# Optimization experiments

Hardware: AMD Instinct MI355X
Metric: run time of the kernel (lower is better)

Reference implementation:

```python
import jax, jax.numpy as jnp
import numpy as np

N_NODES, N_EDGES, N_GRAPHS = 50000, 500000, 64
NODE_D, EDGE_D, GLOB_D = 256, 128, 64
EPS = 1e-5


def setup_inputs() -> dict:
    key = jax.random.key(0)
    ks = jax.random.split(key, 12)
    inp = {
        "x": jax.random.normal(ks[0], (N_NODES, NODE_D), jnp.float32),
        "edge_attr": jax.random.normal(ks[1], (N_EDGES, EDGE_D), jnp.float32),
        "u": jax.random.normal(ks[2], (N_GRAPHS, GLOB_D), jnp.float32),
        "W1": jax.random.normal(ks[3], (NODE_D + EDGE_D, 4 * EDGE_D), jnp.float32) * 0.02,
        "b1": jnp.zeros((4 * EDGE_D,), jnp.float32),
        "W2": jax.random.normal(ks[4], (4 * EDGE_D, EDGE_D), jnp.float32) * 0.02,
        "b2": jnp.zeros((EDGE_D,), jnp.float32),
        "W3": jax.random.normal(ks[5], (NODE_D + EDGE_D + GLOB_D, 4 * NODE_D), jnp.float32) * 0.02,
        "b3": jnp.zeros((4 * NODE_D,), jnp.float32),
        "W4": jax.random.normal(ks[6], (4 * NODE_D, NODE_D), jnp.float32) * 0.02,
        "b4": jnp.zeros((NODE_D,), jnp.float32),
        "gamma": jnp.ones((NODE_D,), jnp.float32),
        "beta": jnp.zeros((NODE_D,), jnp.float32),
        "edge_index": jax.random.randint(ks[7], (2, N_EDGES), 0, N_NODES, jnp.int64 if jax.config.jax_enable_x64 else jnp.int32),
        "batch": jnp.sort(jax.random.randint(ks[8], (N_NODES,), 0, N_GRAPHS, jnp.int64 if jax.config.jax_enable_x64 else jnp.int32)),
    }
    return inp


def reference(x, edge_attr, u, W1, b1, W2, b2, W3, b3, W4, b4, gamma, beta, edge_index, batch):
    row, col = edge_index[0], edge_index[1]
    n = x.shape[0]
    # edge MLP on [x[row] || edge_attr]
    e = jnp.concatenate([x[row], edge_attr], axis=1)            # [E, node+edge]
    e = jnp.maximum(e @ W1 + b1, 0.0) @ W2 + b2                 # [E, edge]
    # scatter-mean by destination node
    s = jax.ops.segment_sum(e, col, num_segments=n)             # [N, edge]
    cnt = jax.ops.segment_sum(jnp.ones((col.shape[0],), x.dtype), col, num_segments=n)
    agg = s / jnp.maximum(cnt, 1.0)[:, None]
    # node update MLP on [x || agg || u[batch]]
    h = jnp.concatenate([x, agg, u[batch]], axis=1)             # [N, node+edge+glob]
    h = jnp.maximum(h @ W3 + b3, 0.0) @ W4 + b4                 # [N, node]
    # residual + layernorm (dropout p=0 -> identity)
    y = h + x
    mu = jnp.mean(y, axis=-1, keepdims=True)
    var = jnp.mean((y - mu) ** 2, axis=-1, keepdims=True)
    return (y - mu) * jax.lax.rsqrt(var + EPS) * gamma + beta
```

## Files before the change

kernel.cpp:

```cpp
#include <hip/hip_runtime.h>
#include <stdint.h>

#define NE 500000
#define NN 50000
#define ND 256
#define ED 128
#define GD 64
#define MAXDEG 64

typedef float f4v __attribute__((ext_vector_type(4)));
typedef short s8v __attribute__((ext_vector_type(8)));
typedef short s4v __attribute__((ext_vector_type(4)));

static __device__ __forceinline__ short f2bf(float f) {
  union { float f; uint32_t u; } v; v.f = f;
  uint32_t r = v.u + 0x7FFFu + ((v.u >> 16) & 1u);
  return (short)(r >> 16);
}
static __device__ __forceinline__ float bf2f(uint32_t u) {
  union { uint32_t u; float f; } v; v.u = u << 16; return v.f;
}

static __device__ __forceinline__ void gload_lds16(const void* g, void* l) {
  __builtin_amdgcn_global_load_lds(
      (const __attribute__((address_space(1))) unsigned int*)g,
      (__attribute__((address_space(3))) unsigned int*)l,
      16, 0, 0);
}

static __device__ __forceinline__ void pack_one(const float* __restrict__ src,
                                                short* __restrict__ dst, int C, int idx) {
  int k = idx / C, c = idx - k * C;
  int ks = k >> 5, kh = (k >> 3) & 3, j = k & 7;
  dst[(((ks * C + c) * 4 + kh) << 3) + j] = f2bf(src[idx]);
}

#define J5 500000
#define J0 3200000
#define J1 196608
#define J2 65536
#define J3 458752
#define J4 262144
__global__ void prep_kernel(const float* __restrict__ x, short* __restrict__ xbf,
                            const float* __restrict__ W1, const float* __restrict__ W2,
                            const float* __restrict__ W3, const float* __restrict__ W4,
                            short* __restrict__ w1p, short* __restrict__ w2p,
                            short* __restrict__ w3p, short* __restrict__ w4p,
                            const int* __restrict__ ecol, unsigned int* __restrict__ cnt,
                            int* __restrict__ elist) {
  int idx = blockIdx.x * blockDim.x + threadIdx.x;
  if (idx < J5) {
    int c = ecol[idx];
    unsigned int slot = atomicAdd(&cnt[c], 1u);
    if (slot < MAXDEG) elist[c * MAXDEG + slot] = idx;
    return;
  }
  idx -= J5;
  if (idx < J0) {
    int i = idx * 4;
    const float4 v = *(const float4*)(x + i);
    s4v o; o[0] = f2bf(v.x); o[1] = f2bf(v.y); o[2] = f2bf(v.z); o[3] = f2bf(v.w);
    *(s4v*)(xbf + i) = o;
    return;
  }
  idx -= J0;
  if (idx < J1) { pack_one(W1, w1p, 512, idx); return; }
  idx -= J1;
  if (idx < J2) { pack_one(W2, w2p, 128, idx); return; }
  idx -= J2;
  if (idx < J3) { pack_one(W3, w3p, 1024, idx); return; }
  idx -= J3;
  if (idx < J4) { pack_one(W4, w4p, 256, idx); return; }
}

__global__ void agg_kernel(const unsigned short* __restrict__ ebuf,
                           const int* __restrict__ elist,
                           const unsigned int* __restrict__ cnt,
                           unsigned short* __restrict__ aggbf) {
  int tid = threadIdx.x;
  int lane = tid & 63;
  int node = blockIdx.x * 4 + (tid >> 6);
  if (node >= NN) return;
  unsigned int deg = cnt[node];
  unsigned int jend = deg < MAXDEG ? deg : MAXDEG;
  const int jg = lane >> 4;
  const int ch = lane & 15;
  float a[8] = {0.f, 0.f, 0.f, 0.f, 0.f, 0.f, 0.f, 0.f};
  const int* el = elist + (size_t)node * MAXDEG;
  for (unsigned int j = jg; j < jend; j += 4) {
    int eid = el[j];
    s8v v = *(const s8v*)(ebuf + (size_t)eid * ED + ch * 8);
    #pragma unroll
    for (int i = 0; i < 8; ++i) a[i] += bf2f((uint32_t)(uint16_t)v[i]);
  }
  #pragma unroll
  for (int d = 16; d < 64; d <<= 1) {
    #pragma unroll
    for (int i = 0; i < 8; ++i) a[i] += __shfl_xor(a[i], d);
  }
  if (jg == 0) {
    float rc = 1.0f / (deg > 0 ? (float)deg : 1.0f);
    s8v o;
    #pragma unroll
    for (int i = 0; i < 8; ++i) o[i] = f2bf(a[i] * rc);
    *(s8v*)(aggbf + (size_t)node * ED + ch * 8) = o;
  }
}

__launch_bounds__(1024, 4)
__global__ void edge_kernel(const short* __restrict__ xbf,
                            const float* __restrict__ edge_attr,
                            const short* __restrict__ w1p,
                            const float* __restrict__ b1,
                            const short* __restrict__ w2p,
                            const float* __restrict__ b2,
                            const int* __restrict__ erow,
                            unsigned short* __restrict__ ebuf) {
  __shared__ __align__(16) short smem[81920];
  char* const Xb = (char*)smem;
  char* const Eb = (char*)smem + 65536;
  char* const Hb = (char*)smem + 98304;
  const int tid = threadIdx.x;
  const int lane = tid & 63;
  const int w = tid >> 6;
  const int lh = lane >> 4;
  const int ll = lane & 15;
  const int e0 = blockIdx.x * 128;

  {
    #pragma unroll
    for (int i = 0; i < 4; ++i) {
      int p = w * 4 + i;
      int row = 2 * p + (lane >> 5);
      int rid = erow[e0 + row];
      int cg = (lane & 31) ^ (row & 7);
      gload_lds16(xbf + (size_t)rid * 256 + cg * 8, Xb + p * 1024);
    }
  }

  #pragma unroll
  for (int it = 0; it < 2; ++it) {
    int id = tid + it * 1024;
    int row = id >> 4, oct = id & 15;
    s8v vals = {0, 0, 0, 0, 0, 0, 0, 0};
    if (e0 + row < NE) {
      const float* p = edge_attr + (size_t)(e0 + row) * ED + oct * 8;
      const float4 v0 = *(const float4*)(p);
      const float4 v1 = *(const float4*)(p + 4);
      vals[0] = f2bf(v0.x); vals[1] = f2bf(v0.y); vals[2] = f2bf(v0.z); vals[3] = f2bf(v0.w);
      vals[4] = f2bf(v1.x); vals[5] = f2bf(v1.y); vals[6] = f2bf(v1.z); vals[7] = f2bf(v1.w);
    }
    *(s8v*)(Eb + row * 256 + ((oct ^ (row & 7)) << 4)) = vals;
  }
  __syncthreads();

  f4v acc1[2][8];
  #pragma unroll
  for (int n = 0; n < 2; ++n)
    #pragma unroll
    for (int m = 0; m < 8; ++m)
      acc1[n][m] = (f4v){0.f, 0.f, 0.f, 0.f};

  for (int ks = 0; ks < 8; ++ks) {
    s8v wf0 = *(const s8v*)(w1p + (((ks * 512 + w * 16 + ll) * 4 + lh) << 3));
    s8v wf1 = *(const s8v*)(w1p + (((ks * 512 + 256 + w * 16 + ll) * 4 + lh) << 3));
    #pragma unroll
    for (int mh = 0; mh < 2; ++mh) {
      s8v hf[4];
      #pragma unroll
      for (int m = 0; m < 4; ++m) {
        int row = 64 * mh + 16 * m + ll;
        int byte = row * 512 + (((ks * 4 + lh) ^ (row & 7)) << 4);
        hf[m] = *(const s8v*)(Xb + byte);
      }
      #pragma unroll
      for (int m = 0; m < 4; ++m) {
        acc1[0][4 * mh + m] = __builtin_amdgcn_mfma_f32_16x16x32_bf16(wf0, hf[m], acc1[0][4 * mh + m], 0, 0, 0);
        acc1[1][4 * mh + m] = __builtin_amdgcn_mfma_f32_16x16x32_bf16(wf1, hf[m], acc1[1][4 * mh + m], 0, 0, 0);
      }
    }
  }
  for (int ks = 8; ks < 12; ++ks) {
    s8v wf0 = *(const s8v*)(w1p + (((ks * 512 + w * 16 + ll) * 4 + lh) << 3));
    s8v wf1 = *(const s8v*)(w1p + (((ks * 512 + 256 + w * 16 + ll) * 4 + lh) << 3));
    #pragma unroll
    for (int mh = 0; mh < 2; ++mh) {
      s8v hf[4];
      #pragma unroll
      for (int m = 0; m < 4; ++m) {
        int row = 64 * mh + 16 * m + ll;
        int byte = row * 256 + ((((ks - 8) * 4 + lh) ^ (row & 7)) << 4);
        hf[m] = *(const s8v*)(Eb + byte);
      }
      #pragma unroll
      for (int m = 0; m < 4; ++m) {
        acc1[0][4 * mh + m] = __builtin_amdgcn_mfma_f32_16x16x32_bf16(wf0, hf[m], acc1[0][4 * mh + m], 0, 0, 0);
        acc1[1][4 * mh + m] = __builtin_amdgcn_mfma_f32_16x16x32_bf16(wf1, hf[m], acc1[1][4 * mh + m], 0, 0, 0);
      }
    }
  }

  {
    int lcb = w * 16 + 4 * lh;
    const float4 bv = *(const float4*)(b1 + lcb);
    #pragma unroll
    for (int m = 0; m < 8; ++m) {
      int row = 16 * m + ll;
      s4v o;
      float v0 = acc1[0][m][0] + bv.x; o[0] = f2bf(v0 > 0.f ? v0 : 0.f);
      float v1 = acc1[0][m][1] + bv.y; o[1] = f2bf(v1 > 0.f ? v1 : 0.f);
      float v2 = acc1[0][m][2] + bv.z; o[2] = f2bf(v2 > 0.f ? v2 : 0.f);
      float v3 = acc1[0][m][3] + bv.w; o[3] = f2bf(v3 > 0.f ? v3 : 0.f);
      int byte = (row * 512 + lcb * 2) ^ ((row & 7) << 4);
      *(s4v*)(Hb + byte) = o;
    }
  }
  __syncthreads();

  f4v acc2[4];
  #pragma unroll
  for (int m = 0; m < 4; ++m)
    acc2[m] = (f4v){0.f, 0.f, 0.f, 0.f};

  {
    int lcb = w * 16 + 4 * lh;
    const float4 bv = *(const float4*)(b1 + 256 + lcb);
    #pragma unroll
    for (int m = 0; m < 8; ++m) {
      int row = 16 * m + ll;
      s4v o;
      float v0 = acc1[1][m][0] + bv.x; o[0] = f2bf(v0 > 0.f ? v0 : 0.f);
      float v1 = acc1[1][m][1] + bv.y; o[1] = f2bf(v1 > 0.f ? v1 : 0.f);
      float v2 = acc1[1][m][2] + bv.z; o[2] = f2bf(v2 > 0.f ? v2 : 0.f);
      float v3 = acc1[1][m][3] + bv.w; o[3] = f2bf(v3 > 0.f ? v3 : 0.f);
      int byte = (row * 512 + lcb * 2) ^ ((row & 7) << 4);
      *(s4v*)(Xb + byte) = o;
    }
  }
  for (int ks = 0; ks < 8; ++ks) {
    s8v wf = *(const s8v*)(w2p + (((ks * 128 + (w & 7) * 16 + ll) * 4 + lh) << 3));
    #pragma unroll
    for (int m = 0; m < 4; ++m) {
      int row = 64 * (w >> 3) + 16 * m + ll;
      int byte = (row * 512 + ks * 64 + lh * 16) ^ ((row & 7) << 4);
      s8v hf = *(const s8v*)(Hb + byte);
      acc2[m] = __builtin_amdgcn_mfma_f32_16x16x32_bf16(wf, hf, acc2[m], 0, 0, 0);
    }
  }
  __syncthreads();

  for (int ks = 8; ks < 16; ++ks) {
    s8v wf = *(const s8v*)(w2p + (((ks * 128 + (w & 7) * 16 + ll) * 4 + lh) << 3));
    #pragma unroll
    for (int m = 0; m < 4; ++m) {
      int row = 64 * (w >> 3) + 16 * m + ll;
      int byte = (row * 512 + (ks - 8) * 64 + lh * 16) ^ ((row & 7) << 4);
      s8v hf = *(const s8v*)(Xb + byte);
      acc2[m] = __builtin_amdgcn_mfma_f32_16x16x32_bf16(wf, hf, acc2[m], 0, 0, 0);
    }
  }

  {
    int cb = (w & 7) * 16 + 4 * lh;
    const float4 bv = *(const float4*)(b2 + cb);
    #pragma unroll
    for (int m = 0; m < 4; ++m) {
      int row = 64 * (w >> 3) + 16 * m + ll;
      int e = e0 + row;
      if (e < NE) {
        s4v o;
        o[0] = f2bf(acc2[m][0] + bv.x);
        o[1] = f2bf(acc2[m][1] + bv.y);
        o[2] = f2bf(acc2[m][2] + bv.z);
        o[3] = f2bf(acc2[m][3] + bv.w);
        *(s4v*)(ebuf + (size_t)e * ED + cb) = o;
      }
    }
  }
}

__launch_bounds__(1024, 4)
__global__ void node_kernel(const float* __restrict__ x,
                            const short* __restrict__ xbf,
                            const float* __restrict__ u,
                            const short* __restrict__ w3p,
                            const float* __restrict__ b3,
                            const short* __restrict__ w4p,
                            const float* __restrict__ b4,
                            const float* __restrict__ gamma,
                            const float* __restrict__ beta,
                            const int* __restrict__ batch,
                            const unsigned short* __restrict__ aggbf,
                            float* __restrict__ out) {
  __shared__ __align__(16) short smem[65536];
  char* const Xn = (char*)smem;
  char* const An = (char*)smem + 32768;
  char* const Un = (char*)smem + 49152;
  char* const H1r = (char*)smem;
  char* const H0r = (char*)smem + 65536;
  const int tid = threadIdx.x;
  const int lane = tid & 63;
  const int w = tid >> 6;
  const int lh = lane >> 4;
  const int ll = lane & 15;
  const int n0 = blockIdx.x * 64;

  {
    #pragma unroll
    for (int i = 0; i < 2; ++i) {
      int p = w * 2 + i;
      int row = 2 * p + (lane >> 5);
      int node = n0 + row; if (node >= NN) node = NN - 1;
      int cg = (lane & 31) ^ (row & 7);
      gload_lds16(xbf + (size_t)node * 256 + cg * 8, Xn + p * 1024);
    }
  }
  {
    int row = tid >> 4, oct = tid & 15;
    s8v v = {0, 0, 0, 0, 0, 0, 0, 0};
    int node = n0 + row;
    if (node < NN) v = *(const s8v*)(aggbf + (size_t)node * ED + oct * 8);
    *(s8v*)(An + row * 256 + ((oct ^ (row & 7)) << 4)) = v;
  }
  if (tid < 512) {
    int row = tid >> 3, oct = tid & 7;
    s8v v = {0, 0, 0, 0, 0, 0, 0, 0};
    int node = n0 + row;
    if (node < NN) {
      const float* up = u + (size_t)batch[node] * GD + oct * 8;
      const float4 v0 = *(const float4*)(up);
      const float4 v1 = *(const float4*)(up + 4);
      v[0] = f2bf(v0.x); v[1] = f2bf(v0.y); v[2] = f2bf(v0.z); v[3] = f2bf(v0.w);
      v[4] = f2bf(v1.x); v[5] = f2bf(v1.y); v[6] = f2bf(v1.z); v[7] = f2bf(v1.w);
    }
    *(s8v*)(Un + row * 128 + ((oct ^ (row & 7)) << 4)) = v;
  }
  __syncthreads();

  f4v acc3[4][4];
  #pragma unroll
  for (int n = 0; n < 4; ++n)
    #pragma unroll
    for (int m = 0; m < 4; ++m)
      acc3[n][m] = (f4v){0.f, 0.f, 0.f, 0.f};

  for (int ks = 0; ks < 14; ++ks) {
    s8v af[4];
    #pragma unroll
    for (int m = 0; m < 4; ++m) {
      int row = 16 * m + ll;
      int byte;
      if (ks < 8)       byte = row * 512 + (((ks * 4 + lh) ^ (row & 7)) << 4);
      else if (ks < 12) byte = row * 256 + ((((ks - 8) * 4 + lh) ^ (row & 7)) << 4);
      else              byte = row * 128 + ((((ks - 12) * 4 + lh) ^ (row & 7)) << 4);
      const char* base = (ks < 8) ? Xn : (ks < 12) ? An : Un;
      af[m] = *(const s8v*)(base + byte);
    }
    #pragma unroll
    for (int n = 0; n < 4; ++n) {
      s8v wf = *(const s8v*)(w3p + (((ks * 1024 + w * 64 + 16 * n + ll) * 4 + lh) << 3));
      #pragma unroll
      for (int m = 0; m < 4; ++m)
        acc3[n][m] = __builtin_amdgcn_mfma_f32_16x16x32_bf16(wf, af[m], acc3[n][m], 0, 0, 0);
    }
  }

  if (w < 8) {
    #pragma unroll
    for (int n = 0; n < 4; ++n) {
      int lc = w * 64 + 16 * n + 4 * lh;
      const float4 bv = *(const float4*)(b3 + lc);
      #pragma unroll
      for (int m = 0; m < 4; ++m) {
        int row = 16 * m + ll;
        s4v o;
        float v0 = acc3[n][m][0] + bv.x; o[0] = f2bf(v0 > 0.f ? v0 : 0.f);
        float v1 = acc3[n][m][1] + bv.y; o[1] = f2bf(v1 > 0.f ? v1 : 0.f);
        float v2 = acc3[n][m][2] + bv.z; o[2] = f2bf(v2 > 0.f ? v2 : 0.f);
        float v3 = acc3[n][m][3] + bv.w; o[3] = f2bf(v3 > 0.f ? v3 : 0.f);
        int byte = (row * 1024 + lc * 2) ^ ((row & 7) << 4);
        *(s4v*)(H0r + byte) = o;
      }
    }
  }
  __syncthreads();

  if (w >= 8) {
    #pragma unroll
    for (int n = 0; n < 4; ++n) {
      int lc = (w - 8) * 64 + 16 * n + 4 * lh;
      const float4 bv = *(const float4*)(b3 + 512 + lc);
      #pragma unroll
      for (int m = 0; m < 4; ++m) {
        int row = 16 * m + ll;
        s4v o;
        float v0 = acc3[n][m][0] + bv.x; o[0] = f2bf(v0 > 0.f ? v0 : 0.f);
        float v1 = acc3[n][m][1] + bv.y; o[1] = f2bf(v1 > 0.f ? v1 : 0.f);
        float v2 = acc3[n][m][2] + bv.z; o[2] = f2bf(v2 > 0.f ? v2 : 0.f);
        float v3 = acc3[n][m][3] + bv.w; o[3] = f2bf(v3 > 0.f ? v3 : 0.f);
        int byte = (row * 1024 + lc * 2) ^ ((row & 7) << 4);
        *(s4v*)(H1r + byte) = o;
      }
    }
  }

  f4v acc4[4];
  #pragma unroll
  for (int m = 0; m < 4; ++m)
    acc4[m] = (f4v){0.f, 0.f, 0.f, 0.f};

  for (int ks = 0; ks < 16; ++ks) {
    s8v wf = *(const s8v*)(w4p + (((ks * 256 + w * 16 + ll) * 4 + lh) << 3));
    #pragma unroll
    for (int m = 0; m < 4; ++m) {
      int row = 16 * m + ll;
      int byte = (row * 1024 + ks * 64 + lh * 16) ^ ((row & 7) << 4);
      s8v hf = *(const s8v*)(H0r + byte);
      acc4[m] = __builtin_amdgcn_mfma_f32_16x16x32_bf16(wf, hf, acc4[m], 0, 0, 0);
    }
  }
  __syncthreads();

  for (int ks = 16; ks < 32; ++ks) {
    s8v wf = *(const s8v*)(w4p + (((ks * 256 + w * 16 + ll) * 4 + lh) << 3));
    #pragma unroll
    for (int m = 0; m < 4; ++m) {
      int row = 16 * m + ll;
      int byte = (row * 1024 + (ks - 16) * 64 + lh * 16) ^ ((row & 7) << 4);
      s8v hf = *(const s8v*)(H1r + byte);
      acc4[m] = __builtin_amdgcn_mfma_f32_16x16x32_bf16(wf, hf, acc4[m], 0, 0, 0);
    }
  }
  __syncthreads();

  float* yb = (float*)smem;
  {
    int cb = w * 16 + 4 * lh;
    const float4 bv = *(const float4*)(b4 + cb);
    #pragma unroll
    for (int m = 0; m < 4; ++m) {
      int row = 16 * m + ll;
      int node = n0 + row;
      float4 xv = {0.f, 0.f, 0.f, 0.f};
      if (node < NN) xv = *(const float4*)(x + (size_t)node * ND + cb);
      f4v o;
      o[0] = acc4[m][0] + bv.x + xv.x;
      o[1] = acc4[m][1] + bv.y + xv.y;
      o[2] = acc4[m][2] + bv.z + xv.z;
      o[3] = acc4[m][3] + bv.w + xv.w;
      *(f4v*)(yb + row * 260 + cb) = o;
    }
  }
  __syncthreads();

  {
    int row = tid >> 4, sub = tid & 15;
    int node = n0 + row;
    float v[16];
    float sum = 0.f, ssq = 0.f;
    #pragma unroll
    for (int i = 0; i < 4; ++i) {
      const float4 t = *(const float4*)(yb + row * 260 + (i * 16 + sub) * 4);
      v[i * 4 + 0] = t.x; v[i * 4 + 1] = t.y; v[i * 4 + 2] = t.z; v[i * 4 + 3] = t.w;
      sum += t.x + t.y + t.z + t.w;
      ssq += t.x * t.x + t.y * t.y + t.z * t.z + t.w * t.w;
    }
    #pragma unroll
    for (int d = 1; d < 16; d <<= 1) {
      sum += __shfl_xor(sum, d);
      ssq += __shfl_xor(ssq, d);
    }
    float mu = sum * (1.f / 256.f);
    float var = ssq * (1.f / 256.f) - mu * mu;
    float rstd = rsqrtf(var + 1e-5f);
    if (node < NN) {
      #pragma unroll
      for (int i = 0; i < 4; ++i) {
        int c = (i * 16 + sub) * 4;
        const float4 g = *(const float4*)(gamma + c);
        const float4 be = *(const float4*)(beta + c);
        float4 o;
        o.x = (v[i * 4 + 0] - mu) * rstd * g.x + be.x;
        o.y = (v[i * 4 + 1] - mu) * rstd * g.y + be.y;
        o.z = (v[i * 4 + 2] - mu) * rstd * g.z + be.z;
        o.w = (v[i * 4 + 3] - mu) * rstd * g.w + be.w;
        *(float4*)(out + (size_t)node * ND + c) = o;
      }
    }
  }
}

extern "C" void kernel_launch(void* const* d_in, const int* in_sizes, int n_in,
                              void* d_out, int out_size, void* d_ws, size_t ws_size,
                              hipStream_t stream) {
  const float* x    = (const float*)d_in[0];
  const float* ea   = (const float*)d_in[1];
  const float* u    = (const float*)d_in[2];
  const float* W1   = (const float*)d_in[3];
  const float* b1   = (const float*)d_in[4];
  const float* W2   = (const float*)d_in[5];
  const float* b2   = (const float*)d_in[6];
  const float* W3   = (const float*)d_in[7];
  const float* b3   = (const float*)d_in[8];
  const float* W4   = (const float*)d_in[9];
  const float* b4   = (const float*)d_in[10];
  const float* gamma = (const float*)d_in[11];
  const float* beta  = (const float*)d_in[12];
  const int* eidx   = (const int*)d_in[13];
  const int* batch  = (const int*)d_in[14];
  float* out = (float*)d_out;

  char* p = (char*)d_ws;
  size_t off = 0;
  auto take = [&](size_t n) { char* r = p + off; off = (off + n + 255) & ~(size_t)255; return r; };
  short* xbf = (short*)take((size_t)NN * ND * 2);
  short* w1p = (short*)take((size_t)384 * 512 * 2);
  short* w2p = (short*)take((size_t)512 * 128 * 2);
  short* w3p = (short*)take((size_t)448 * 1024 * 2);
  short* w4p = (short*)take((size_t)1024 * 256 * 2);
  unsigned int* cnt = (unsigned int*)take((size_t)NN * 4);
  int* elist = (int*)take((size_t)NN * MAXDEG * 4);
  unsigned short* aggbf = (unsigned short*)take((size_t)NN * ED * 2);
  unsigned short* ebuf = (unsigned short*)take((size_t)NE * ED * 2);

  const int* erow = eidx;
  const int* ecol = eidx + NE;

  hipMemsetAsync(cnt, 0, (size_t)NN * 4, stream);
  {
    const int total = J5 + J0 + J1 + J2 + J3 + J4;
    prep_kernel<<<(total + 255) / 256, 256, 0, stream>>>(x, xbf, W1, W2, W3, W4,
                                                         w1p, w2p, w3p, w4p,
                                                         ecol, cnt, elist);
  }
  edge_kernel<<<(NE + 127) / 128, 1024, 0, stream>>>(xbf, ea, w1p, b1, w2p, b2, erow, ebuf);
  agg_kernel<<<(NN + 3) / 4, 256, 0, stream>>>(ebuf, elist, cnt, aggbf);
  node_kernel<<<(NN + 63) / 64, 1024, 0, stream>>>(x, xbf, u, w3p, b3, w4p, b4,
                                                   gamma, beta, batch, aggbf, out);
}
```

Before: 587.6 us.

## Switch edge MLP to 32x32x16 MFMA tiles with repacked weights

Rewrites both edge-MLP GEMMs to use 32x32x16 bf16 MFMA instead of 16x16x32, with W1/W2 repacked to the matching K-split layout. Each wave now owns 32 output columns across all 128 edges in GEMM1, and a 32x32 tile in GEMM2. The larger tiles halve the weight-fragment loads and the LDS fragment reads per FLOP, and give better MFMA throughput per instruction. In exchange, the epilogue mapping and bias indexing change, and the hidden-layer write split between Hb and Xb now depends on which waves hold which column halves.

```diff
diff --git a/kernel.cpp b/kernel.cpp
--- a/kernel.cpp
+++ b/kernel.cpp
@@ -9,6 +9,7 @@
 #define MAXDEG 64
 
 typedef float f4v __attribute__((ext_vector_type(4)));
+typedef float f16v __attribute__((ext_vector_type(16)));
 typedef short s8v __attribute__((ext_vector_type(8)));
 typedef short s4v __attribute__((ext_vector_type(4)));
 
@@ -33,6 +34,12 @@
   int k = idx / C, c = idx - k * C;
   int ks = k >> 5, kh = (k >> 3) & 3, j = k & 7;
   dst[(((ks * C + c) * 4 + kh) << 3) + j] = f2bf(src[idx]);
+}
+static __device__ __forceinline__ void pack32_one(const float* __restrict__ src,
+                                                  short* __restrict__ dst, int C, int idx) {
+  int k = idx / C, c = idx - k * C;
+  int ks = k >> 4, kh = (k >> 3) & 1, j = k & 7;
+  dst[(((ks * C + c) * 2 + kh) << 3) + j] = f2bf(src[idx]);
 }
 
 #define J5 500000
@@ -64,9 +71,9 @@
     return;
   }
   idx -= J0;
-  if (idx < J1) { pack_one(W1, w1p, 512, idx); return; }
+  if (idx < J1) { pack32_one(W1, w1p, 512, idx); return; }
   idx -= J1;
-  if (idx < J2) { pack_one(W2, w2p, 128, idx); return; }
+  if (idx < J2) { pack32_one(W2, w2p, 128, idx); return; }
   idx -= J2;
   if (idx < J3) { pack_one(W3, w3p, 1024, idx); return; }
   idx -= J3;
@@ -123,8 +130,8 @@
   const int tid = threadIdx.x;
   const int lane = tid & 63;
   const int w = tid >> 6;
-  const int lh = lane >> 4;
-  const int ll = lane & 15;
+  const int l31 = lane & 31;
+  const int lg = lane >> 5;
   const int e0 = blockIdx.x * 128;
 
   {
@@ -137,7 +144,6 @@
       gload_lds16(xbf + (size_t)rid * 256 + cg * 8, Xb + p * 1024);
     }
   }
-
   #pragma unroll
   for (int it = 0; it < 2; ++it) {
     int id = tid + it * 1024;
@@ -154,126 +160,109 @@
   }
   __syncthreads();
 
-  f4v acc1[2][8];
+  f16v acc1[4];
   #pragma unroll
-  for (int n = 0; n < 2; ++n)
-    #pragma unroll
-    for (int m = 0; m < 8; ++m)
-      acc1[n][m] = (f4v){0.f, 0.f, 0.f, 0.f};
-
-  for (int ks = 0; ks < 8; ++ks) {
-    s8v wf0 = *(const s8v*)(w1p + (((ks * 512 + w * 16 + ll) * 4 + lh) << 3));
-    s8v wf1 = *(const s8v*)(w1p + (((ks * 512 + 256 + w * 16 + ll) * 4 + lh) << 3));
-    #pragma unroll
-    for (int mh = 0; mh < 2; ++mh) {
-      s8v hf[4];
-      #pragma unroll
-      for (int m = 0; m < 4; ++m) {
-        int row = 64 * mh + 16 * m + ll;
-        int byte = row * 512 + (((ks * 4 + lh) ^ (row & 7)) << 4);
-        hf[m] = *(const s8v*)(Xb + byte);
+  for (int et = 0; et < 4; ++et)
+    #pragma unroll
+    for (int r = 0; r < 16; ++r)
+      acc1[et][r] = 0.f;
+
+  for (int ks = 0; ks < 16; ++ks) {
+    s8v wf = *(const s8v*)(w1p + (((ks * 512 + w * 32 + l31) * 2 + lg) << 3));
+    #pragma unroll
+    for (int et = 0; et < 4; ++et) {
+      int row = et * 32 + l31;
+      int byte = row * 512 + (((ks * 2 + lg) ^ (row & 7)) << 4);
+      s8v hf = *(const s8v*)(Xb + byte);
+      acc1[et] = __builtin_amdgcn_mfma_f32_32x32x16_bf16(wf, hf, acc1[et], 0, 0, 0);
+    }
+  }
+  for (int ks = 16; ks < 24; ++ks) {
+    s8v wf = *(const s8v*)(w1p + (((ks * 512 + w * 32 + l31) * 2 + lg) << 3));
+    #pragma unroll
+    for (int et = 0; et < 4; ++et) {
+      int row = et * 32 + l31;
+      int byte = row * 256 + ((((ks - 16) * 2 + lg) ^ (row & 7)) << 4);
+      s8v hf = *(const s8v*)(Eb + byte);
+      acc1[et] = __builtin_amdgcn_mfma_f32_32x32x16_bf16(wf, hf, acc1[et], 0, 0, 0);
+    }
+  }
+
+  if (w < 8) {
+    #pragma unroll
+    for (int et = 0; et < 4; ++et) {
+      int row = et * 32 + l31;
+      #pragma unroll
+      for (int q = 0; q < 4; ++q) {
+        int cg = w * 32 + 8 * q + 4 * lg;
+        const float4 bv = *(const float4*)(b1 + cg);
+        s4v o;
+        float v0 = acc1[et][4 * q + 0] + bv.x; o[0] = f2bf(v0 > 0.f ? v0 : 0.f);
+        float v1 = acc1[et][4 * q + 1] + bv.y; o[1] = f2bf(v1 > 0.f ? v1 : 0.f);
+        float v2 = acc1[et][4 * q + 2] + bv.z; o[2] = f2bf(v2 > 0.f ? v2 : 0.f);
+        float v3 = acc1[et][4 * q + 3] + bv.w; o[3] = f2bf(v3 > 0.f ? v3 : 0.f);
+        int byte = (row * 512 + cg * 2) ^ ((row & 7) << 4);
+        *(s4v*)(Hb + byte) = o;
       }
-      #pragma unroll
-      for (int m = 0; m < 4; ++m) {
-        acc1[0][4 * mh + m] = __builtin_amdgcn_mfma_f32_16x16x32_bf16(wf0, hf[m], acc1[0][4 * mh + m], 0, 0, 0);
-        acc1[1][4 * mh + m] = __builtin_amdgcn_mfma_f32_16x16x32_bf16(wf1, hf[m], acc1[1][4 * mh + m], 0, 0, 0);
+    }
+  }
+  __syncthreads();
+
+  if (w >= 8) {
+    #pragma unroll
+    for (int et = 0; et < 4; ++et) {
+      int row = et * 32 + l31;
+      #pragma unroll
+      for (int q = 0; q < 4; ++q) {
+        int cg = w * 32 + 8 * q + 4 * lg;
+        const float4 bv = *(const float4*)(b1 + cg);
+        int lc = cg - 256;
+        s4v o;
+        float v0 = acc1[et][4 * q + 0] + bv.x; o[0] = f2bf(v0 > 0.f ? v0 : 0.f);
+        float v1 = acc1[et][4 * q + 1] + bv.y; o[1] = f2bf(v1 > 0.f ? v1 : 0.f);
+        float v2 = acc1[et][4 * q + 2] + bv.z; o[2] = f2bf(v2 > 0.f ? v2 : 0.f);
+        float v3 = acc1[et][4 * q + 3] + bv.w; o[3] = f2bf(v3 > 0.f ? v3 : 0.f);
+        int byte = (row * 512 + lc * 2) ^ ((row & 7) << 4);
+        *(s4v*)(Xb + byte) = o;
       }
     }
   }
-  for (int ks = 8; ks < 12; ++ks) {
-    s8v wf0 = *(const s8v*)(w1p + (((ks * 512 + w * 16 + ll) * 4 + lh) << 3));
-    s8v wf1 = *(const s8v*)(w1p + (((ks * 512 + 256 + w * 16 + ll) * 4 + lh) << 3));
-    #pragma unroll
-    for (int mh = 0; mh < 2; ++mh) {
-      s8v hf[4];
-      #pragma unroll
-      for (int m = 0; m < 4; ++m) {
-        int row = 64 * mh + 16 * m + ll;
-        int byte = row * 256 + ((((ks - 8) * 4 + lh) ^ (row & 7)) << 4);
-        hf[m] = *(const s8v*)(Eb + byte);
-      }
-      #pragma unroll
-      for (int m = 0; m < 4; ++m) {
-        acc1[0][4 * mh + m] = __builtin_amdgcn_mfma_f32_16x16x32_bf16(wf0, hf[m], acc1[0][4 * mh + m], 0, 0, 0);
-        acc1[1][4 * mh + m] = __builtin_amdgcn_mfma_f32_16x16x32_bf16(wf1, hf[m], acc1[1][4 * mh + m], 0, 0, 0);
-      }
-    }
-  }
-
-  {
-    int lcb = w * 16 + 4 * lh;
-    const float4 bv = *(const float4*)(b1 + lcb);
-    #pragma unroll
-    for (int m = 0; m < 8; ++m) {
-      int row = 16 * m + ll;
-      s4v o;
-      float v0 = acc1[0][m][0] + bv.x; o[0] = f2bf(v0 > 0.f ? v0 : 0.f);
-      float v1 = acc1[0][m][1] + bv.y; o[1] = f2bf(v1 > 0.f ? v1 : 0.f);
-      float v2 = acc1[0][m][2] + bv.z; o[2] = f2bf(v2 > 0.f ? v2 : 0.f);
-      float v3 = acc1[0][m][3] + bv.w; o[3] = f2bf(v3 > 0.f ? v3 : 0.f);
-      int byte = (row * 512 + lcb * 2) ^ ((row & 7) << 4);
-      *(s4v*)(Hb + byte) = o;
-    }
-  }
-  __syncthreads();
-
-  f4v acc2[4];
+
+  f16v acc2;
   #pragma unroll
-  for (int m = 0; m < 4; ++m)
-    acc2[m] = (f4v){0.f, 0.f, 0.f, 0.f};
-
-  {
-    int lcb = w * 16 + 4 * lh;
-    const float4 bv = *(const float4*)(b1 + 256 + lcb);
-    #pragma unroll
-    for (int m = 0; m < 8; ++m) {
-      int row = 16 * m + ll;
-      s4v o;
-      float v0 = acc1[1][m][0] + bv.x; o[0] = f2bf(v0 > 0.f ? v0 : 0.f);
-      float v1 = acc1[1][m][1] + bv.y; o[1] = f2bf(v1 > 0.f ? v1 : 0.f);
-      float v2 = acc1[1][m][2] + bv.z; o[2] = f2bf(v2 > 0.f ? v2 : 0.f);
-      float v3 = acc1[1][m][3] + bv.w; o[3] = f2bf(v3 > 0.f ? v3 : 0.f);
-      int byte = (row * 512 + lcb * 2) ^ ((row & 7) << 4);
-      *(s4v*)(Xb + byte) = o;
-    }
-  }
-  for (int ks = 0; ks < 8; ++ks) {
-    s8v wf = *(const s8v*)(w2p + (((ks * 128 + (w & 7) * 16 + ll) * 4 + lh) << 3));
-    #pragma unroll
-    for (int m = 0; m < 4; ++m) {
-      int row = 64 * (w >> 3) + 16 * m + ll;
-      int byte = (row * 512 + ks * 64 + lh * 16) ^ ((row & 7) << 4);
-      s8v hf = *(const s8v*)(Hb + byte);
-      acc2[m] = __builtin_amdgcn_mfma_f32_16x16x32_bf16(wf, hf, acc2[m], 0, 0, 0);
-    }
-  }
-  __syncthreads();
-
-  for (int ks = 8; ks < 16; ++ks) {
-    s8v wf = *(const s8v*)(w2p + (((ks * 128 + (w & 7) * 16 + ll) * 4 + lh) << 3));
-    #pragma unroll
-    for (int m = 0; m < 4; ++m) {
-      int row = 64 * (w >> 3) + 16 * m + ll;
-      int byte = (row * 512 + (ks - 8) * 64 + lh * 16) ^ ((row & 7) << 4);
-      s8v hf = *(const s8v*)(Xb + byte);
-      acc2[m] = __builtin_amdgcn_mfma_f32_16x16x32_bf16(wf, hf, acc2[m], 0, 0, 0);
-    }
-  }
-
-  {
-    int cb = (w & 7) * 16 + 4 * lh;
-    const float4 bv = *(const float4*)(b2 + cb);
-    #pragma unroll
-    for (int m = 0; m < 4; ++m) {
-      int row = 64 * (w >> 3) + 16 * m + ll;
-      int e = e0 + row;
-      if (e < NE) {
+  for (int r = 0; r < 16; ++r) acc2[r] = 0.f;
+
+  const int erow0 = (w >> 2) * 32;
+  for (int ks = 0; ks < 16; ++ks) {
+    s8v wf = *(const s8v*)(w2p + (((ks * 128 + (w & 3) * 32 + l31) * 2 + lg) << 3));
+    int row = erow0 + l31;
+    int byte = row * 512 + (((ks * 2 + lg) ^ (row & 7)) << 4);
+    s8v hf = *(const s8v*)(Hb + byte);
+    acc2 = __builtin_amdgcn_mfma_f32_32x32x16_bf16(wf, hf, acc2, 0, 0, 0);
+  }
+  __syncthreads();
+
+  for (int ks = 16; ks < 32; ++ks) {
+    s8v wf = *(const s8v*)(w2p + (((ks * 128 + (w & 3) * 32 + l31) * 2 + lg) << 3));
+    int row = erow0 + l31;
+    int byte = row * 512 + ((((ks - 16) * 2 + lg) ^ (row & 7)) << 4);
+    s8v hf = *(const s8v*)(Xb + byte);
+    acc2 = __builtin_amdgcn_mfma_f32_32x32x16_bf16(wf, hf, acc2, 0, 0, 0);
+  }
+
+  {
+    int e = e0 + erow0 + l31;
+    if (e < NE) {
+      #pragma unroll
+      for (int q = 0; q < 4; ++q) {
+        int c = (w & 3) * 32 + 8 * q + 4 * lg;
+        const float4 bv = *(const float4*)(b2 + c);
         s4v o;
-        o[0] = f2bf(acc2[m][0] + bv.x);
-        o[1] = f2bf(acc2[m][1] + bv.y);
-        o[2] = f2bf(acc2[m][2] + bv.z);
-        o[3] = f2bf(acc2[m][3] + bv.w);
-        *(s4v*)(ebuf + (size_t)e * ED + cb) = o;
+        o[0] = f2bf(acc2[4 * q + 0] + bv.x);
+        o[1] = f2bf(acc2[4 * q + 1] + bv.y);
+        o[2] = f2bf(acc2[4 * q + 2] + bv.z);
+        o[3] = f2bf(acc2[4 * q + 3] + bv.w);
+        *(s4v*)(ebuf + (size_t)e * ED + c) = o;
       }
     }
   }
```

New measurement: 629.2 us. +7.1%, slower.
